# Performance work log

Measured on AMD Instinct MI355X. Metric: run time of the kernel, lower is better.

Reference implementation:

```python
import jax, jax.numpy as jnp
import numpy as np
import math

B, S, D, H = 2, 2048, 1024, 16
DH = D // H

def setup_inputs() -> dict:
    key0 = jax.random.key(0)
    ks = jax.random.split(key0, 12)
    s = 1.0 / math.sqrt(D)
    return {
        "query": jax.random.normal(ks[0], (B, S, D), jnp.float32),
        "key": jax.random.normal(ks[1], (B, S, D), jnp.float32),
        "value": jax.random.normal(ks[2], (B, S, D), jnp.float32),
        "mask": jax.random.randint(ks[3], (B, 1, S, S), 0, 2, jnp.int32),
        "Wq": jax.random.normal(ks[4], (D, D), jnp.float32) * s,
        "bq": jnp.zeros((D,), jnp.float32),
        "Wk": jax.random.normal(ks[5], (D, D), jnp.float32) * s,
        "bk": jnp.zeros((D,), jnp.float32),
        "Wv": jax.random.normal(ks[6], (D, D), jnp.float32) * s,
        "bv": jnp.zeros((D,), jnp.float32),
        "Wo": jax.random.normal(ks[7], (D, D), jnp.float32) * s,
        "bo": jnp.zeros((D,), jnp.float32),
    }

def reference(query, key, value, mask, Wq, bq, Wk, bk, Wv, bv, Wo, bo):
    # Linear projections (torch Linear: x @ W.T + b)
    q = query @ Wq.T + bq
    k = key @ Wk.T + bk
    v = value @ Wv.T + bv
    # [B, S, D] -> [B, H, S, DH]
    q = q.reshape(B, S, H, DH).transpose(0, 2, 1, 3)
    k = k.reshape(B, S, H, DH).transpose(0, 2, 1, 3)
    v = v.reshape(B, S, H, DH).transpose(0, 2, 1, 3)
    # scaled dot-product attention with explicit [B,H,S,S] scores
    score = jnp.einsum('bhqd,bhkd->bhqk', q, k) / math.sqrt(DH)
    score = jnp.where(mask == 0, jnp.float32(-1e9), score)
    attn = jax.nn.softmax(score, axis=-1)
    out = jnp.einsum('bhqk,bhkd->bhqd', attn, v)
    out = out.transpose(0, 2, 1, 3).reshape(B, S, D)
    return out @ Wo.T + bo
```

## Files before the change

### kernel.cpp

```cpp
#include <hip/hip_runtime.h>
#include <hip/hip_bf16.h>

typedef __attribute__((ext_vector_type(4))) float f32x4;
typedef __attribute__((ext_vector_type(8))) short bf16x8;
typedef __attribute__((ext_vector_type(4))) short s16x4;
typedef __attribute__((ext_vector_type(4))) unsigned int u32x4;
typedef unsigned short ushort_t;
typedef unsigned int u32;
typedef unsigned long long u64;

constexpr int B = 2, S = 2048, D = 1024, H = 16, DH = 64;

__device__ __forceinline__ ushort_t f2bf(float f) {
    union { float f; unsigned int i; } v; v.f = f;
    unsigned int r = v.i + 0x7fffu + ((v.i >> 16) & 1u);
    return (ushort_t)(r >> 16);
}

__device__ __forceinline__ float fast_exp2(float x) {
#if __has_builtin(__builtin_amdgcn_exp2f)
    return __builtin_amdgcn_exp2f(x);
#else
    return exp2f(x);
#endif
}

__device__ __forceinline__ u32 pack_hi16(u32 b1, u32 b0) {
#if __has_builtin(__builtin_amdgcn_perm)
    return __builtin_amdgcn_perm(b1, b0, 0x07060302u);
#else
    return (b1 & 0xffff0000u) | (b0 >> 16);
#endif
}

__device__ __forceinline__ void gload_lds16(const void* g, void* l) {
    __builtin_amdgcn_global_load_lds(
        (const __attribute__((address_space(1))) unsigned int*)g,
        (__attribute__((address_space(3))) unsigned int*)l,
        16, 0, 0);
}

__global__ __launch_bounds__(256) void cvt_f32_bf16(
    const float* __restrict__ in, ushort_t* __restrict__ out, int n)
{
    int i = (blockIdx.x * 256 + threadIdx.x) * 4;
    if (i >= n) return;
    f32x4 v = *(const f32x4*)(in + i);
    s16x4 o;
    for (int j = 0; j < 4; ++j) o[j] = (short)f2bf(v[j]);
    *(s16x4*)(out + i) = o;
}

__global__ __launch_bounds__(256) void cvt3_f32_bf16(
    const float* __restrict__ a0, const float* __restrict__ a1,
    const float* __restrict__ a2, ushort_t* __restrict__ out, int n)
{
    const float* in = blockIdx.y == 0 ? a0 : (blockIdx.y == 1 ? a1 : a2);
    int i = (blockIdx.x * 256 + threadIdx.x) * 4;
    if (i >= n) return;
    f32x4 v = *(const f32x4*)(in + i);
    s16x4 o;
    for (int j = 0; j < 4; ++j) o[j] = (short)f2bf(v[j]);
    *(s16x4*)(out + (size_t)blockIdx.y * n + i) = o;
}

__global__ __launch_bounds__(256) void cvt4_f32_bf16(
    const float* __restrict__ a0, const float* __restrict__ a1,
    const float* __restrict__ a2, const float* __restrict__ a3,
    ushort_t* __restrict__ out, int n)
{
    const float* in = blockIdx.y == 0 ? a0 : (blockIdx.y == 1 ? a1 :
                      (blockIdx.y == 2 ? a2 : a3));
    int i = (blockIdx.x * 256 + threadIdx.x) * 4;
    if (i >= n) return;
    f32x4 v = *(const f32x4*)(in + i);
    s16x4 o;
    for (int j = 0; j < 4; ++j) o[j] = (short)f2bf(v[j]);
    *(s16x4*)(out + (size_t)blockIdx.y * n + i) = o;
}

__global__ __launch_bounds__(256) void pack_mask(
    const int* __restrict__ mask, u64* __restrict__ pm)
{
    const int wave_g = (blockIdx.x * 256 + threadIdx.x) >> 6;
    const int lane = threadIdx.x & 63;
    for (int w = 0; w < 16; ++w) {
        size_t idx = (size_t)wave_g * 16 + w;
        int mv = mask[idx * 64 + lane];
        u64 bal = __ballot(mv != 0);
        if (lane == 0) {
            int t = (int)(idx & 31);
            int q = (int)((idx >> 5) & (S - 1));
            int b = (int)(idx >> 16);
            pm[((size_t)b * 32 + t) * S + q] = bal;
        }
    }
}

__global__ __launch_bounds__(256) void transpose_v(
    const ushort_t* __restrict__ Vw, ushort_t* __restrict__ Vt)
{
    __shared__ ushort_t T[64][80];
    const int st = blockIdx.x, bh = blockIdx.y;
    const int b = bh / H, h = bh % H;
    const int tid = threadIdx.x;
    const int r = tid >> 3, c = tid & 7;
    for (int p = 0; p < 2; ++p) {
        int s = p * 32 + r;
        bf16x8 v = *(const bf16x8*)(Vw + (size_t)(b * S + st * 64 + s) * D + h * DH + c * 8);
        *(bf16x8*)(&T[s][c * 8]) = v;
    }
    __syncthreads();
    const int q0q = (c >> 2) * 8 + (c & 3);
    for (int p = 0; p < 2; ++p) {
        int d = p * 32 + r;
        bf16x8 o;
        for (int j = 0; j < 4; ++j) o[j]     = (short)T[q0q * 4 + j][d];
        for (int j = 0; j < 4; ++j) o[4 + j] = (short)T[(q0q + 4) * 4 + j][d];
        *(bf16x8*)(Vt + (size_t)((b * H + h) * DH + d) * S + st * 64 + c * 8) = o;
    }
}

template <typename OutT>
__device__ __forceinline__ void gemm_body(
    const ushort_t* __restrict__ Ag,
    const ushort_t* __restrict__ Wg,
    const float* __restrict__ bias,
    OutT* __restrict__ Cg,
    int M, int N, int K,
    ushort_t* As, ushort_t* Bs)
{
    constexpr int BK = 64;
    const int tid  = threadIdx.x;
    const int wid  = tid >> 6;
    const int lane = tid & 63;
    const int m0 = blockIdx.x * 128;
    const int n0 = blockIdx.y * 128;
    const int wr = wid >> 1, wc = wid & 1;

    const int lrow = lane & 15;
    const int lk8  = (lane >> 4) * 8;
    const int srow  = lane >> 3;
    const int sbyte = (lane & 7) * 16;

    f32x4 acc[4][4] = {};

    for (int k0 = 0; k0 < K; k0 += BK) {
        for (int c = 0; c < 4; ++c) {
            int r0 = wid * 32 + c * 8;
            gload_lds16((const char*)(Ag + (size_t)(m0 + r0 + srow) * K + k0) + sbyte,
                        (char*)As + r0 * 128);
            gload_lds16((const char*)(Wg + (size_t)(n0 + r0 + srow) * K + k0) + sbyte,
                        (char*)Bs + r0 * 128);
        }
        __syncthreads();

        for (int kk = 0; kk < BK; kk += 32) {
            bf16x8 af[4], bfr[4];
            for (int i = 0; i < 4; ++i) {
                af[i]  = *(const bf16x8*)(As + (wr * 64 + i * 16 + lrow) * BK + kk + lk8);
                bfr[i] = *(const bf16x8*)(Bs + (wc * 64 + i * 16 + lrow) * BK + kk + lk8);
            }
            for (int i = 0; i < 4; ++i)
                for (int j = 0; j < 4; ++j)
                    acc[i][j] = __builtin_amdgcn_mfma_f32_16x16x32_bf16(
                        af[i], bfr[j], acc[i][j], 0, 0, 0);
        }
        __syncthreads();
    }

    const int crow0 = (lane >> 4) * 4;
    const int ccol  = lane & 15;
    for (int j = 0; j < 4; ++j) {
        int col = n0 + wc * 64 + j * 16 + ccol;
        float bv = bias[col];
        for (int i = 0; i < 4; ++i) {
            for (int r = 0; r < 4; ++r) {
                int row = m0 + wr * 64 + i * 16 + crow0 + r;
                float val = acc[i][j][r] + bv;
                if constexpr (__is_same(OutT, float))
                    Cg[(size_t)row * N + col] = val;
                else
                    Cg[(size_t)row * N + col] = f2bf(val);
            }
        }
    }
}

template <typename OutT>
__global__ __launch_bounds__(256, 2) void gemm_bt_bias(
    const ushort_t* __restrict__ Ag, const ushort_t* __restrict__ Wg,
    const float* __restrict__ bias, OutT* __restrict__ Cg,
    int M, int N, int K)
{
    __shared__ ushort_t As[128 * 64];
    __shared__ ushort_t Bs[128 * 64];
    gemm_body<OutT>(Ag, Wg, bias, Cg, M, N, K, As, Bs);
}

__global__ __launch_bounds__(256, 2) void gemm_qkv(
    const ushort_t* __restrict__ X3,
    const ushort_t* __restrict__ W4,
    const float* __restrict__ b0, const float* __restrict__ b1,
    const float* __restrict__ b2,
    ushort_t* __restrict__ QKV,
    int M, int N, int K)
{
    __shared__ ushort_t As[128 * 64];
    __shared__ ushort_t Bs[128 * 64];
    const int z = blockIdx.z;
    const float* bias = z == 0 ? b0 : (z == 1 ? b1 : b2);
    gemm_body<ushort_t>(X3 + (size_t)z * M * K, W4 + (size_t)z * N * K,
                        bias, QKV + (size_t)z * M * N, M, N, K, As, Bs);
}

__global__ __launch_bounds__(256, 4) void attn_kernel(
    const ushort_t* __restrict__ Q,
    const ushort_t* __restrict__ Kt,
    const ushort_t* __restrict__ Vt,
    const u64* __restrict__ pmask,
    ushort_t* __restrict__ O)
{
    constexpr int KVBLK = 64;
    constexpr int NT = S / KVBLK;
    constexpr float C1 = 0.18033688f;
    constexpr float C2 = 17.31234049f;
    __shared__ ushort_t Ks[KVBLK * DH];
    __shared__ ushort_t Vs[KVBLK * DH];

    const int tid  = threadIdx.x;
    const int wid  = tid >> 6;
    const int lane = tid & 63;
    const int qt = blockIdx.x;
    const int bh = blockIdx.y;
    const int b = bh / H, h = bh % H;
    const int q0 = qt * 64 + wid * 16;

    const int lq   = lane & 15;
    const int hi   = lane >> 4;
    const int lk8  = hi * 8;
    const int srow = lane >> 3;
    const int sbyte = (((lane & 7) ^ srow) & 7) * 16;

    bf16x8 qf[2];
    #pragma unroll
    for (int kk = 0; kk < 2; ++kk)
        qf[kk] = *(const bf16x8*)(Q + (size_t)(b * S + q0 + lq) * D + h * DH + kk * 32 + lk8);

    f32x4 oacc[4] = {};
    f32x4 ps = {};
    const u32x4 onesw = {0x3f803f80u, 0x3f803f80u, 0x3f803f80u, 0x3f803f80u};
    const bf16x8 onesf = __builtin_bit_cast(bf16x8, onesw);

    const u64* pmrow = pmask + (size_t)b * 32 * S + q0 + lq;
    const ushort_t* Vtb = Vt + (size_t)(b * H + h) * DH * S;

    for (int t = 0; t < NT; ++t) {
        const int kv0 = t * KVBLK;
        #pragma unroll
        for (int c = 0; c < 2; ++c) {
            int r0 = wid * 16 + c * 8;
            gload_lds16((const char*)(Kt + (size_t)(b * S + kv0 + r0 + srow) * D + h * DH) + sbyte,
                        (char*)Ks + r0 * 128);
            gload_lds16((const char*)(Vtb + (size_t)(r0 + srow) * S + kv0) + sbyte,
                        (char*)Vs + r0 * 128);
        }
        const u64 mw = pmrow[(size_t)t * S];
        __syncthreads();

        f32x4 sc[4] = {};
        #pragma unroll
        for (int kk = 0; kk < 2; ++kk) {
            const int chunk = ((kk * 4 + hi) ^ (lq & 7)) * 8;
            #pragma unroll
            for (int ni = 0; ni < 4; ++ni) {
                bf16x8 kf = *(const bf16x8*)(Ks + (ni * 16 + lq) * 64 + chunk);
                sc[ni] = __builtin_amdgcn_mfma_f32_16x16x32_bf16(kf, qf[kk], sc[ni], 0, 0, 0);
            }
        }

        const u32 lo32 = (u32)mw;
        const u32 hi32 = (u32)(mw >> 32);
        u32 paw[8];
        #pragma unroll
        for (int ni = 0; ni < 4; ++ni) {
            const u32 word = (ni < 2) ? lo32 : hi32;
            const int base = (ni & 1) * 16 + hi * 4;
            u32 pb[4];
            #pragma unroll
            for (int r = 0; r < 4; ++r) {
                float p = fast_exp2(__builtin_fmaf(sc[ni][r], C1, -C2));
                int mbit = ((int)(word << (31 - (base + r)))) >> 31;
                pb[r] = __builtin_bit_cast(u32, p) & (u32)mbit;
            }
            paw[ni * 2]     = pack_hi16(pb[1], pb[0]);
            paw[ni * 2 + 1] = pack_hi16(pb[3], pb[2]);
        }

        #pragma unroll
        for (int kk = 0; kk < 2; ++kk) {
            u32x4 pv = {paw[kk * 4], paw[kk * 4 + 1], paw[kk * 4 + 2], paw[kk * 4 + 3]};
            bf16x8 paf = __builtin_bit_cast(bf16x8, pv);
            ps = __builtin_amdgcn_mfma_f32_16x16x32_bf16(paf, onesf, ps, 0, 0, 0);
            const int chunk = ((kk * 4 + hi) ^ (lq & 7)) * 8;
            #pragma unroll
            for (int di = 0; di < 4; ++di) {
                bf16x8 vf = *(const bf16x8*)(Vs + (di * 16 + lq) * 64 + chunk);
                oacc[di] = __builtin_amdgcn_mfma_f32_16x16x32_bf16(paf, vf, oacc[di], 0, 0, 0);
            }
        }
        __syncthreads();
    }

    float inv[4];
    #pragma unroll
    for (int r = 0; r < 4; ++r) inv[r] = 1.0f / ps[r];
    #pragma unroll
    for (int di = 0; di < 4; ++di) {
        #pragma unroll
        for (int r = 0; r < 4; ++r) {
            float v = oacc[di][r] * inv[r];
            O[(size_t)(b * S + q0 + hi * 4 + r) * D + h * DH + di * 16 + lq] = f2bf(v);
        }
    }
}

extern "C" void kernel_launch(void* const* d_in, const int* in_sizes, int n_in,
                              void* d_out, int out_size, void* d_ws, size_t ws_size,
                              hipStream_t stream) {
    const float* query = (const float*)d_in[0];
    const float* key   = (const float*)d_in[1];
    const float* value = (const float*)d_in[2];
    const int*   mask  = (const int*)d_in[3];
    const float* Wq = (const float*)d_in[4];
    const float* bq = (const float*)d_in[5];
    const float* Wk = (const float*)d_in[6];
    const float* bk = (const float*)d_in[7];
    const float* Wv = (const float*)d_in[8];
    const float* bv = (const float*)d_in[9];
    const float* Wo = (const float*)d_in[10];
    const float* bo = (const float*)d_in[11];
    float* out = (float*)d_out;

    const int M = B * S;
    const int NX = M * D;
    const int NW = D * D;

    char* ws = (char*)d_ws;
    const size_t MB = 1024 * 1024;
    dim3 gblk(M / 128, D / 128);
    const int gcX = NX / (4 * 256);
    const int gcW = NW / (4 * 256);
    const int pmBlocks = (B * S * (S / 64)) / (16 * 4);

    if (ws_size >= 58 * MB) {
        ushort_t* X3  = (ushort_t*)(ws);
        ushort_t* Vtb = (ushort_t*)(ws);
        ushort_t* Ow  = (ushort_t*)(ws + 8 * MB);
        ushort_t* W4  = (ushort_t*)(ws + 24 * MB);
        ushort_t* QKV = (ushort_t*)(ws + 32 * MB);
        ushort_t* Qw = QKV, *Kw = QKV + NX, *Vw = QKV + 2 * (size_t)NX;
        u64* pm = (u64*)(ws + 56 * MB);

        cvt3_f32_bf16<<<dim3(gcX, 3), 256, 0, stream>>>(query, key, value, X3, NX);
        cvt4_f32_bf16<<<dim3(gcW, 4), 256, 0, stream>>>(Wq, Wk, Wv, Wo, W4, NW);
        pack_mask<<<pmBlocks, 256, 0, stream>>>(mask, pm);

        gemm_qkv<<<dim3(M / 128, D / 128, 3), 256, 0, stream>>>(
            X3, W4, bq, bk, bv, QKV, M, D, D);

        transpose_v<<<dim3(S / 64, B * H), 256, 0, stream>>>(Vw, Vtb);
        attn_kernel<<<dim3(S / 64, B * H), 256, 0, stream>>>(Qw, Kw, Vtb, pm, Ow);

        gemm_bt_bias<float><<<gblk, 256, 0, stream>>>(Ow, W4 + 3 * (size_t)NW, bo, out, M, D, D);
    } else {
        ushort_t* Xb = (ushort_t*)(ws);
        ushort_t* Vtb = (ushort_t*)(ws);
        ushort_t* Wb = (ushort_t*)(ws + 8  * MB);
        u64*      pm = (u64*)(ws + 8 * MB);
        ushort_t* Qw = (ushort_t*)(ws + 16 * MB);
        ushort_t* Kw = (ushort_t*)(ws + 24 * MB);
        ushort_t* Vw = (ushort_t*)(ws + 32 * MB);
        ushort_t* Ow = (ushort_t*)(ws + 40 * MB);

        cvt_f32_bf16<<<gcX, 256, 0, stream>>>(query, Xb, NX);
        cvt_f32_bf16<<<gcW, 256, 0, stream>>>(Wq, Wb, NW);
        gemm_bt_bias<ushort_t><<<gblk, 256, 0, stream>>>(Xb, Wb, bq, Qw, M, D, D);

        cvt_f32_bf16<<<gcX, 256, 0, stream>>>(key, Xb, NX);
        cvt_f32_bf16<<<gcW, 256, 0, stream>>>(Wk, Wb, NW);
        gemm_bt_bias<ushort_t><<<gblk, 256, 0, stream>>>(Xb, Wb, bk, Kw, M, D, D);

        cvt_f32_bf16<<<gcX, 256, 0, stream>>>(value, Xb, NX);
        cvt_f32_bf16<<<gcW, 256, 0, stream>>>(Wv, Wb, NW);
        gemm_bt_bias<ushort_t><<<gblk, 256, 0, stream>>>(Xb, Wb, bv, Vw, M, D, D);

        transpose_v<<<dim3(S / 64, B * H), 256, 0, stream>>>(Vw, Vtb);
        pack_mask<<<pmBlocks, 256, 0, stream>>>(mask, pm);

        attn_kernel<<<dim3(S / 64, B * H), 256, 0, stream>>>(Qw, Kw, Vtb, pm, Ow);

        cvt_f32_bf16<<<gcW, 256, 0, stream>>>(Wo, Wb, NW);
        gemm_bt_bias<float><<<gblk, 256, 0, stream>>>(Ow, Wb, bo, out, M, D, D);
    }
}
```

Measured before the change: 148.4 us.

## Fuse V transpose into QKV GEMM epilogue, shrink GEMM N-tile, prioritize attention MFMAs

Drops the separate transpose_v kernel by having the QKV GEMM write the V projection directly in the transposed, permuted layout the attention kernel reads. The GEMM tile shrinks from 128x128 to 128x64, which doubles the block count and raises the occupancy target to 4. The attention kernel wraps its MFMA sections in s_setprio so matrix work gets issue priority. The cost is lower data reuse per GEMM tile and scattered 8-byte stores in the V epilogue.

```diff
diff --git a/kernel.cpp b/kernel.cpp
--- a/kernel.cpp
+++ b/kernel.cpp
@@ -122,20 +122,21 @@
 }
 
 template <typename OutT>
-__device__ __forceinline__ void gemm_body(
+__device__ __forceinline__ void gemm_body64(
     const ushort_t* __restrict__ Ag,
     const ushort_t* __restrict__ Wg,
     const float* __restrict__ bias,
     OutT* __restrict__ Cg,
+    ushort_t* __restrict__ VtOut,
     int M, int N, int K,
-    ushort_t* As, ushort_t* Bs)
+    ushort_t* As, ushort_t* Bs, bool vepi)
 {
     constexpr int BK = 64;
     const int tid  = threadIdx.x;
     const int wid  = tid >> 6;
     const int lane = tid & 63;
     const int m0 = blockIdx.x * 128;
-    const int n0 = blockIdx.y * 128;
+    const int n0 = blockIdx.y * 64;
     const int wr = wid >> 1, wc = wid & 1;
 
     const int lrow = lane & 15;
@@ -143,75 +144,113 @@
     const int srow  = lane >> 3;
     const int sbyte = (lane & 7) * 16;
 
-    f32x4 acc[4][4] = {};
+    f32x4 acc[4][2] = {};
 
     for (int k0 = 0; k0 < K; k0 += BK) {
+        #pragma unroll
         for (int c = 0; c < 4; ++c) {
             int r0 = wid * 32 + c * 8;
             gload_lds16((const char*)(Ag + (size_t)(m0 + r0 + srow) * K + k0) + sbyte,
                         (char*)As + r0 * 128);
+        }
+        #pragma unroll
+        for (int c = 0; c < 2; ++c) {
+            int r0 = wid * 16 + c * 8;
             gload_lds16((const char*)(Wg + (size_t)(n0 + r0 + srow) * K + k0) + sbyte,
                         (char*)Bs + r0 * 128);
         }
         __syncthreads();
 
+        #pragma unroll
         for (int kk = 0; kk < BK; kk += 32) {
-            bf16x8 af[4], bfr[4];
-            for (int i = 0; i < 4; ++i) {
+            bf16x8 af[4], bfr[2];
+            #pragma unroll
+            for (int i = 0; i < 4; ++i)
                 af[i]  = *(const bf16x8*)(As + (wr * 64 + i * 16 + lrow) * BK + kk + lk8);
-                bfr[i] = *(const bf16x8*)(Bs + (wc * 64 + i * 16 + lrow) * BK + kk + lk8);
-            }
+            #pragma unroll
+            for (int j = 0; j < 2; ++j)
+                bfr[j] = *(const bf16x8*)(Bs + (wc * 32 + j * 16 + lrow) * BK + kk + lk8);
+            #pragma unroll
             for (int i = 0; i < 4; ++i)
-                for (int j = 0; j < 4; ++j)
+                #pragma unroll
+                for (int j = 0; j < 2; ++j)
                     acc[i][j] = __builtin_amdgcn_mfma_f32_16x16x32_bf16(
                         af[i], bfr[j], acc[i][j], 0, 0, 0);
         }
         __syncthreads();
     }
 
-    const int crow0 = (lane >> 4) * 4;
+    const int hi    = lane >> 4;
+    const int crow0 = hi * 4;
     const int ccol  = lane & 15;
-    for (int j = 0; j < 4; ++j) {
-        int col = n0 + wc * 64 + j * 16 + ccol;
-        float bv = bias[col];
-        for (int i = 0; i < 4; ++i) {
-            for (int r = 0; r < 4; ++r) {
-                int row = m0 + wr * 64 + i * 16 + crow0 + r;
-                float val = acc[i][j][r] + bv;
-                if constexpr (__is_same(OutT, float))
-                    Cg[(size_t)row * N + col] = val;
-                else
-                    Cg[(size_t)row * N + col] = f2bf(val);
+
+    if (vepi) {
+        const int hv = n0 >> 6;
+        #pragma unroll
+        for (int j = 0; j < 2; ++j) {
+            int dcol = wc * 32 + j * 16 + ccol;
+            float bv = bias[n0 + dcol];
+            #pragma unroll
+            for (int i = 0; i < 4; ++i) {
+                int row = m0 + wr * 64 + i * 16 + crow0;
+                int b = row >> 11;
+                int s = row & (S - 1);
+                int sbase = s & ~63;
+                int pos = ((i >> 1) * 4 + hi) * 8 + (i & 1) * 4;
+                s16x4 o;
+                #pragma unroll
+                for (int r = 0; r < 4; ++r) o[r] = (short)f2bf(acc[i][j][r] + bv);
+                *(s16x4*)(VtOut + ((size_t)(b * H + hv) * DH + dcol) * S + sbase + pos) = o;
             }
         }
+    } else {
+        #pragma unroll
+        for (int j = 0; j < 2; ++j) {
+            int col = n0 + wc * 32 + j * 16 + ccol;
+            float bv = bias[col];
+            #pragma unroll
+            for (int i = 0; i < 4; ++i) {
+                #pragma unroll
+                for (int r = 0; r < 4; ++r) {
+                    int row = m0 + wr * 64 + i * 16 + crow0 + r;
+                    float val = acc[i][j][r] + bv;
+                    if constexpr (__is_same(OutT, float))
+                        Cg[(size_t)row * N + col] = val;
+                    else
+                        Cg[(size_t)row * N + col] = f2bf(val);
+                }
+            }
+        }
     }
 }
 
 template <typename OutT>
-__global__ __launch_bounds__(256, 2) void gemm_bt_bias(
+__global__ __launch_bounds__(256, 4) void gemm_bt_bias(
     const ushort_t* __restrict__ Ag, const ushort_t* __restrict__ Wg,
     const float* __restrict__ bias, OutT* __restrict__ Cg,
     int M, int N, int K)
 {
     __shared__ ushort_t As[128 * 64];
-    __shared__ ushort_t Bs[128 * 64];
-    gemm_body<OutT>(Ag, Wg, bias, Cg, M, N, K, As, Bs);
-}
-
-__global__ __launch_bounds__(256, 2) void gemm_qkv(
+    __shared__ ushort_t Bs[64 * 64];
+    gemm_body64<OutT>(Ag, Wg, bias, Cg, nullptr, M, N, K, As, Bs, false);
+}
+
+__global__ __launch_bounds__(256, 4) void gemm_qkv(
     const ushort_t* __restrict__ X3,
     const ushort_t* __restrict__ W4,
     const float* __restrict__ b0, const float* __restrict__ b1,
     const float* __restrict__ b2,
     ushort_t* __restrict__ QKV,
+    ushort_t* __restrict__ Vt,
     int M, int N, int K)
 {
     __shared__ ushort_t As[128 * 64];
-    __shared__ ushort_t Bs[128 * 64];
+    __shared__ ushort_t Bs[64 * 64];
     const int z = blockIdx.z;
     const float* bias = z == 0 ? b0 : (z == 1 ? b1 : b2);
-    gemm_body<ushort_t>(X3 + (size_t)z * M * K, W4 + (size_t)z * N * K,
-                        bias, QKV + (size_t)z * M * N, M, N, K, As, Bs);
+    gemm_body64<ushort_t>(X3 + (size_t)z * M * K, W4 + (size_t)z * N * K,
+                          bias, QKV + (size_t)z * M * N, Vt,
+                          M, N, K, As, Bs, z == 2);
 }
 
 __global__ __launch_bounds__(256, 4) void attn_kernel(
@@ -269,6 +308,7 @@
         __syncthreads();
 
         f32x4 sc[4] = {};
+        __builtin_amdgcn_s_setprio(1);
         #pragma unroll
         for (int kk = 0; kk < 2; ++kk) {
             const int chunk = ((kk * 4 + hi) ^ (lq & 7)) * 8;
@@ -278,6 +318,7 @@
                 sc[ni] = __builtin_amdgcn_mfma_f32_16x16x32_bf16(kf, qf[kk], sc[ni], 0, 0, 0);
             }
         }
+        __builtin_amdgcn_s_setprio(0);
 
         const u32 lo32 = (u32)mw;
         const u32 hi32 = (u32)(mw >> 32);
@@ -297,6 +338,7 @@
             paw[ni * 2 + 1] = pack_hi16(pb[3], pb[2]);
         }
 
+        __builtin_amdgcn_s_setprio(1);
         #pragma unroll
         for (int kk = 0; kk < 2; ++kk) {
             u32x4 pv = {paw[kk * 4], paw[kk * 4 + 1], paw[kk * 4 + 2], paw[kk * 4 + 3]};
@@ -309,6 +351,7 @@
                 oacc[di] = __builtin_amdgcn_mfma_f32_16x16x32_bf16(paf, vf, oacc[di], 0, 0, 0);
             }
         }
+        __builtin_amdgcn_s_setprio(0);
         __syncthreads();
     }
 
@@ -348,28 +391,27 @@
 
     char* ws = (char*)d_ws;
     const size_t MB = 1024 * 1024;
-    dim3 gblk(M / 128, D / 128);
+    dim3 gblk(M / 128, D / 64);
     const int gcX = NX / (4 * 256);
     const int gcW = NW / (4 * 256);
     const int pmBlocks = (B * S * (S / 64)) / (16 * 4);
 
     if (ws_size >= 58 * MB) {
         ushort_t* X3  = (ushort_t*)(ws);
-        ushort_t* Vtb = (ushort_t*)(ws);
         ushort_t* Ow  = (ushort_t*)(ws + 8 * MB);
         ushort_t* W4  = (ushort_t*)(ws + 24 * MB);
         ushort_t* QKV = (ushort_t*)(ws + 32 * MB);
-        ushort_t* Qw = QKV, *Kw = QKV + NX, *Vw = QKV + 2 * (size_t)NX;
+        ushort_t* Qw = QKV, *Kw = QKV + NX;
+        ushort_t* Vtb = QKV + 2 * (size_t)NX;
         u64* pm = (u64*)(ws + 56 * MB);
 
         cvt3_f32_bf16<<<dim3(gcX, 3), 256, 0, stream>>>(query, key, value, X3, NX);
         cvt4_f32_bf16<<<dim3(gcW, 4), 256, 0, stream>>>(Wq, Wk, Wv, Wo, W4, NW);
         pack_mask<<<pmBlocks, 256, 0, stream>>>(mask, pm);
 
-        gemm_qkv<<<dim3(M / 128, D / 128, 3), 256, 0, stream>>>(
-            X3, W4, bq, bk, bv, QKV, M, D, D);
-
-        transpose_v<<<dim3(S / 64, B * H), 256, 0, stream>>>(Vw, Vtb);
+        gemm_qkv<<<dim3(M / 128, D / 64, 3), 256, 0, stream>>>(
+            X3, W4, bq, bk, bv, QKV, Vtb, M, D, D);
+
         attn_kernel<<<dim3(S / 64, B * H), 256, 0, stream>>>(Qw, Kw, Vtb, pm, Ow);
 
         gemm_bt_bias<float><<<gblk, 256, 0, stream>>>(Ow, W4 + 3 * (size_t)NW, bo, out, M, D, D);
```

Result: no change. 150.3 us (+1.3%).
